# Kernel tuning notes

Measured on AMD Instinct MI355X. Metric: run time of the kernel, lower is better.

Reference implementation:

```python
import jax, jax.numpy as jnp
import numpy as np

N_NODES = 100000
D_IN = 256
D_OUT = 128
N_EDGES = 1600000
KEEP_PROB = 0.5  # tf.nn.dropout(input, 1 - 0.5) -> rate = 0.5


def setup_inputs() -> dict:
    key = jax.random.key(0)
    k_x, k_mask, k_w, k_row, k_col, k_ew = jax.random.split(key, 6)
    x = jax.random.normal(k_x, (N_NODES, D_IN), dtype=jnp.float32)
    # Deterministic scaled dropout keep-mask: Bernoulli(keep)/keep
    u = jax.random.uniform(k_mask, (N_NODES, D_IN), dtype=jnp.float32)
    dropout_mask = (u < KEEP_PROB).astype(jnp.float32) / KEEP_PROB
    kernel = jax.random.normal(k_w, (D_IN, D_OUT), dtype=jnp.float32) * (1.0 / np.sqrt(D_IN))
    edge_row = jax.random.randint(k_row, (N_EDGES,), 0, N_NODES, dtype=jnp.int32)
    edge_col = jax.random.randint(k_col, (N_EDGES,), 0, N_NODES, dtype=jnp.int32)
    edge_weight = jax.random.uniform(k_ew, (N_EDGES,), dtype=jnp.float32)
    return {"x": x, "dropout_mask": dropout_mask, "kernel": kernel,
            "edge_row": edge_row, "edge_col": edge_col, "edge_weight": edge_weight}


def reference(x, dropout_mask, kernel, edge_row, edge_col, edge_weight):
    # dropout (mask already scaled by 1/keep_prob)
    h = x * dropout_mask                      # [N, D_IN]
    # dense projection
    h = h @ kernel                            # [N, D_OUT]
    # sparse (COO) adjacency @ dense: out[r] += w_e * h[c] for each edge (r, c)
    msgs = edge_weight[:, None] * h[edge_col]            # [E, D_OUT]
    agg = jax.ops.segment_sum(msgs, edge_row, num_segments=N_NODES)  # [N, D_OUT]
    # act=True -> relu
    return jax.nn.relu(agg)
```

## Files before the change

kernel.cpp:

```cpp
#include <hip/hip_runtime.h>

constexpr int NN = 100000;
constexpr int DI = 256;
constexpr int DO = 128;
constexpr int NE = 1600000;

constexpr int BROWS = 128;
constexpr int NBK   = (NN + BROWS - 1) / BROWS;
constexpr int TILE  = 8192;
constexpr int CAP   = 2688;

typedef __bf16 bf16x8 __attribute__((ext_vector_type(8)));
typedef float  f32x4  __attribute__((ext_vector_type(4)));

__device__ inline unsigned short f2bf(float f) {
    union { float f; unsigned u; } v; v.f = f;
    return (unsigned short)((v.u + 0x7FFF + ((v.u >> 16) & 1)) >> 16);
}
__device__ inline float bf2f(unsigned u16) {
    union { unsigned u; float f; } v; v.u = u16 << 16;
    return v.f;
}

__global__ __launch_bounds__(256)
void wt_kernel(const float* __restrict__ W, unsigned short* __restrict__ Wt) {
    __shared__ float t[32][33];
    const int tx = threadIdx.x & 31, ty = threadIdx.x >> 5;
    const int k0 = (blockIdx.x >> 2) * 32, n0 = (blockIdx.x & 3) * 32;
#pragma unroll
    for (int i = 0; i < 32; i += 8)
        t[ty + i][tx] = W[(size_t)(k0 + ty + i) * DO + n0 + tx];
    __syncthreads();
#pragma unroll
    for (int i = 0; i < 32; i += 8)
        Wt[(size_t)(n0 + ty + i) * DI + k0 + tx] = f2bf(t[tx][ty + i]);
}

__global__ __launch_bounds__(256)
void gemm_kernel(const float* __restrict__ x, const float* __restrict__ mask,
                 const unsigned short* __restrict__ Wt,
                 unsigned short* __restrict__ h) {
    __shared__ unsigned short As[128][72];
    __shared__ unsigned short Bs[128][72];
    const int tid  = threadIdx.x;
    const int lane = tid & 63;
    const int w    = tid >> 6;
    const int m0   = blockIdx.x * 128;
    const int mw   = w * 32;
    const int l15  = lane & 15;
    const int l4   = lane >> 4;

    f32x4 acc[2][8];
#pragma unroll
    for (int rt = 0; rt < 2; ++rt)
#pragma unroll
        for (int ct = 0; ct < 8; ++ct) acc[rt][ct] = (f32x4){0.f, 0.f, 0.f, 0.f};

    for (int kc = 0; kc < DI; kc += 64) {
        {
            const int kl = (tid & 15) * 4;
#pragma unroll
            for (int p = 0; p < 8; ++p) {
                const int r = p * 16 + (tid >> 4);
                float4 xv = make_float4(0.f, 0.f, 0.f, 0.f);
                float4 mv = make_float4(0.f, 0.f, 0.f, 0.f);
                if (m0 + r < NN) {
                    xv = *(const float4*)(x    + (size_t)(m0 + r) * DI + kc + kl);
                    mv = *(const float4*)(mask + (size_t)(m0 + r) * DI + kc + kl);
                }
                ushort4 pk;
                pk.x = f2bf(xv.x * mv.x); pk.y = f2bf(xv.y * mv.y);
                pk.z = f2bf(xv.z * mv.z); pk.w = f2bf(xv.w * mv.w);
                *(ushort4*)&As[r][kl] = pk;
            }
        }
        {
            const int kl = (tid & 7) * 8;
#pragma unroll
            for (int p = 0; p < 4; ++p) {
                const int n = p * 32 + (tid >> 3);
                *(uint4*)&Bs[n][kl] =
                    *(const uint4*)(Wt + (size_t)n * DI + kc + kl);
            }
        }
        __syncthreads();
#pragma unroll
        for (int ks = 0; ks < 2; ++ks) {
            const int ko = ks * 32 + l4 * 8;
            bf16x8 a0 = *(const bf16x8*)&As[mw + l15][ko];
            bf16x8 a1 = *(const bf16x8*)&As[mw + 16 + l15][ko];
#pragma unroll
            for (int ct = 0; ct < 8; ++ct) {
                bf16x8 b = *(const bf16x8*)&Bs[ct * 16 + l15][ko];
                acc[0][ct] = __builtin_amdgcn_mfma_f32_16x16x32_bf16(a0, b, acc[0][ct], 0, 0, 0);
                acc[1][ct] = __builtin_amdgcn_mfma_f32_16x16x32_bf16(a1, b, acc[1][ct], 0, 0, 0);
            }
        }
        __syncthreads();
    }
#pragma unroll
    for (int rt = 0; rt < 2; ++rt)
#pragma unroll
        for (int ct = 0; ct < 8; ++ct)
#pragma unroll
            for (int reg = 0; reg < 4; ++reg) {
                const int row = m0 + mw + rt * 16 + l4 * 4 + reg;
                if (row < NN)
                    h[(size_t)row * DO + ct * 16 + l15] = f2bf(acc[rt][ct][reg]);
            }
}

__global__ __launch_bounds__(256)
void bhist_kernel(const int* __restrict__ erow, int* __restrict__ bcnt) {
    __shared__ int cnt[NBK];
    const int t = threadIdx.x;
    for (int k = t; k < NBK; k += 256) cnt[k] = 0;
    __syncthreads();
    for (int e = blockIdx.x * 256 + t; e < NE; e += 256 * 256)
        atomicAdd(&cnt[erow[e] >> 7], 1);
    __syncthreads();
    for (int k = t; k < NBK; k += 256) {
        const int c = cnt[k];
        if (c) atomicAdd(&bcnt[k], c);
    }
}

__global__ __launch_bounds__(1024)
void bscan_kernel(const int* __restrict__ bcnt, int* __restrict__ bstart,
                  int* __restrict__ bcursor) {
    __shared__ int wsum[16];
    const int t = threadIdx.x, lane = t & 63, wid = t >> 6;
    const int c = (t < NBK) ? bcnt[t] : 0;
    int v = c;
#pragma unroll
    for (int off = 1; off < 64; off <<= 1) {
        const int n = __shfl_up(v, off, 64);
        if (lane >= off) v += n;
    }
    if (lane == 63) wsum[wid] = v;
    __syncthreads();
    int p = 0;
#pragma unroll
    for (int i = 0; i < 16; ++i)
        if (i < wid) p += wsum[i];
    const int excl = p + v - c;
    if (t <= NBK) bstart[t] = excl;
    if (t < NBK)  bcursor[t] = excl;
}

__global__ __launch_bounds__(256)
void part_kernel(const int* __restrict__ erow, const int* __restrict__ ecol,
                 const float* __restrict__ ew, int* __restrict__ bcursor,
                 int2* __restrict__ csr) {
    __shared__ int cnt[NBK];
    __shared__ int base[NBK];
    const int t  = threadIdx.x;
    const int e0 = blockIdx.x * TILE;
    for (int k = t; k < NBK; k += 256) cnt[k] = 0;
    __syncthreads();
    for (int k = 0; k < TILE; k += 256) {
        const int e = e0 + k + t;
        if (e < NE) atomicAdd(&cnt[erow[e] >> 7], 1);
    }
    __syncthreads();
    for (int k = t; k < NBK; k += 256) {
        const int c = cnt[k];
        base[k] = c ? atomicAdd(&bcursor[k], c) : 0;
        cnt[k] = 0;
    }
    __syncthreads();
    for (int k = 0; k < TILE; k += 256) {
        const int e = e0 + k + t;
        if (e < NE) {
            const int row = erow[e];
            const int bk  = row >> 7;
            const int pos = atomicAdd(&cnt[bk], 1);
            int2 v;
            v.x = ((row & 127) << 17) | ecol[e];
            v.y = __float_as_int(ew[e]);
            csr[base[bk] + pos] = v;
        }
    }
}

__global__ __launch_bounds__(256)
void bgather_kernel(const unsigned short* __restrict__ h,
                    const int* __restrict__ bstart,
                    const int2* __restrict__ csr, float* __restrict__ out) {
    __shared__ int2 se[CAP];
    __shared__ int  s_cnt[BROWS];
    __shared__ int  s_start[BROWS + 1];
    __shared__ int  wtot;
    const int b = blockIdx.x, t = threadIdx.x;
    const int start = bstart[b], n = bstart[b + 1] - start;

    if (t < BROWS) s_cnt[t] = 0;
    __syncthreads();
    for (int j = t; j < n; j += 256)
        atomicAdd(&s_cnt[((unsigned)csr[start + j].x) >> 17], 1);
    __syncthreads();
    const int lane = t & 63;
    int c = 0;
    if (t < BROWS) c = s_cnt[t];
    int v = c;
#pragma unroll
    for (int off = 1; off < 64; off <<= 1) {
        const int nn = __shfl_up(v, off, 64);
        if (lane >= off) v += nn;
    }
    if (t == 63) wtot = v;
    __syncthreads();
    if (t < BROWS) {
        const int excl = v - c + (t >= 64 ? wtot : 0);
        s_start[t] = excl;
        s_cnt[t]   = excl;
    }
    if (t == 0) s_start[BROWS] = n;
    __syncthreads();
    for (int j = t; j < n; j += 256) {
        const int2 cw = csr[start + j];
        const int  pos = atomicAdd(&s_cnt[((unsigned)cw.x) >> 17], 1);
        se[pos] = cw;
    }
    __syncthreads();

    const int l16 = t & 15, g = t >> 4;
    const int row0 = b * BROWS;
#pragma unroll
    for (int rp = 0; rp < 8; ++rp) {
        const int r  = rp * 16 + g;
        const int gr = row0 + r;
        const int rs = s_start[r], re = s_start[r + 1];
        float acc[8];
#pragma unroll
        for (int i = 0; i < 8; ++i) acc[i] = 0.f;
        int j = rs;
        for (; j + 2 <= re; j += 2) {
            const int2 cw0 = se[j], cw1 = se[j + 1];
            const float w0 = __int_as_float(cw0.y);
            const float w1 = __int_as_float(cw1.y);
            const uint4 q0 = *(const uint4*)(h + (size_t)(cw0.x & 0x1FFFF) * DO + l16 * 8);
            const uint4 q1 = *(const uint4*)(h + (size_t)(cw1.x & 0x1FFFF) * DO + l16 * 8);
            const unsigned* u0 = (const unsigned*)&q0;
            const unsigned* u1 = (const unsigned*)&q1;
#pragma unroll
            for (int i = 0; i < 4; ++i) {
                acc[2 * i + 0] += w0 * bf2f(u0[i] & 0xFFFF) + w1 * bf2f(u1[i] & 0xFFFF);
                acc[2 * i + 1] += w0 * bf2f(u0[i] >> 16)    + w1 * bf2f(u1[i] >> 16);
            }
        }
        if (j < re) {
            const int2 cw = se[j];
            const float w = __int_as_float(cw.y);
            const uint4 q = *(const uint4*)(h + (size_t)(cw.x & 0x1FFFF) * DO + l16 * 8);
            const unsigned* u = (const unsigned*)&q;
#pragma unroll
            for (int i = 0; i < 4; ++i) {
                acc[2 * i + 0] += w * bf2f(u[i] & 0xFFFF);
                acc[2 * i + 1] += w * bf2f(u[i] >> 16);
            }
        }
        if (gr < NN) {
            float* op = out + (size_t)gr * DO + l16 * 8;
            *(float4*)(op + 0) = make_float4(fmaxf(acc[0], 0.f), fmaxf(acc[1], 0.f),
                                             fmaxf(acc[2], 0.f), fmaxf(acc[3], 0.f));
            *(float4*)(op + 4) = make_float4(fmaxf(acc[4], 0.f), fmaxf(acc[5], 0.f),
                                             fmaxf(acc[6], 0.f), fmaxf(acc[7], 0.f));
        }
    }
}

extern "C" void kernel_launch(void* const* d_in, const int* in_sizes, int n_in,
                              void* d_out, int out_size, void* d_ws, size_t ws_size,
                              hipStream_t stream) {
    const float* x    = (const float*)d_in[0];
    const float* mask = (const float*)d_in[1];
    const float* W    = (const float*)d_in[2];
    const int*   erow = (const int*)d_in[3];
    const int*   ecol = (const int*)d_in[4];
    const float* ew   = (const float*)d_in[5];
    float* out = (float*)d_out;

    char* p = (char*)d_ws;
    unsigned short* h  = (unsigned short*)p;  p += (size_t)NN * DO * 2;
    unsigned short* Wt = (unsigned short*)p;  p += (size_t)DO * DI * 2;
    int* bcnt    = (int*)p;                   p += 3200;
    int* bstart  = (int*)p;                   p += 3200;
    int* bcursor = (int*)p;                   p += 3200;
    int2* csr    = (int2*)p;

    hipMemsetAsync(bcnt, 0, NBK * sizeof(int), stream);

    wt_kernel<<<32, 256, 0, stream>>>(W, Wt);
    gemm_kernel<<<(NN + 127) / 128, 256, 0, stream>>>(x, mask, Wt, h);
    bhist_kernel<<<256, 256, 0, stream>>>(erow, bcnt);
    bscan_kernel<<<1, 1024, 0, stream>>>(bcnt, bstart, bcursor);
    part_kernel<<<(NE + TILE - 1) / TILE, 256, 0, stream>>>(erow, ecol, ew,
                                                            bcursor, csr);
    bgather_kernel<<<NBK, 256, 0, stream>>>(h, bstart, csr, out);
}
```

Measured before the change: 413.6 us.

## Prefetch GEMM tiles, drop histogram/scan via fixed-capacity buckets, widen gather blocks

Result: faster. 389.6 us (-5.8%).

```diff
diff --git a/kernel.cpp b/kernel.cpp
--- a/kernel.cpp
+++ b/kernel.cpp
@@ -40,39 +40,43 @@
 void gemm_kernel(const float* __restrict__ x, const float* __restrict__ mask,
                  const unsigned short* __restrict__ Wt,
                  unsigned short* __restrict__ h) {
-    __shared__ unsigned short As[128][72];
+    __shared__ unsigned short As[64][72];
     __shared__ unsigned short Bs[128][72];
     const int tid  = threadIdx.x;
     const int lane = tid & 63;
     const int w    = tid >> 6;
-    const int m0   = blockIdx.x * 128;
-    const int mw   = w * 32;
+    const int m0   = blockIdx.x * 64;
+    const int mw   = w * 16;
     const int l15  = lane & 15;
     const int l4   = lane >> 4;
 
-    f32x4 acc[2][8];
-#pragma unroll
-    for (int rt = 0; rt < 2; ++rt)
-#pragma unroll
-        for (int ct = 0; ct < 8; ++ct) acc[rt][ct] = (f32x4){0.f, 0.f, 0.f, 0.f};
+    f32x4 acc[8];
+#pragma unroll
+    for (int ct = 0; ct < 8; ++ct) acc[ct] = (f32x4){0.f, 0.f, 0.f, 0.f};
+
+    const int lr = tid >> 4;
+    const int lk = (tid & 15) * 4;
+
+    float4 xv[4], mv[4];
+    const float4 z4 = make_float4(0.f, 0.f, 0.f, 0.f);
+
+#pragma unroll
+    for (int p = 0; p < 4; ++p) {
+        const int r = m0 + p * 16 + lr;
+        if (r < NN) {
+            xv[p] = *(const float4*)(x    + (size_t)r * DI + lk);
+            mv[p] = *(const float4*)(mask + (size_t)r * DI + lk);
+        } else { xv[p] = z4; mv[p] = z4; }
+    }
 
     for (int kc = 0; kc < DI; kc += 64) {
-        {
-            const int kl = (tid & 15) * 4;
-#pragma unroll
-            for (int p = 0; p < 8; ++p) {
-                const int r = p * 16 + (tid >> 4);
-                float4 xv = make_float4(0.f, 0.f, 0.f, 0.f);
-                float4 mv = make_float4(0.f, 0.f, 0.f, 0.f);
-                if (m0 + r < NN) {
-                    xv = *(const float4*)(x    + (size_t)(m0 + r) * DI + kc + kl);
-                    mv = *(const float4*)(mask + (size_t)(m0 + r) * DI + kc + kl);
-                }
-                ushort4 pk;
-                pk.x = f2bf(xv.x * mv.x); pk.y = f2bf(xv.y * mv.y);
-                pk.z = f2bf(xv.z * mv.z); pk.w = f2bf(xv.w * mv.w);
-                *(ushort4*)&As[r][kl] = pk;
-            }
+        __syncthreads();
+#pragma unroll
+        for (int p = 0; p < 4; ++p) {
+            ushort4 pk;
+            pk.x = f2bf(xv[p].x * mv[p].x); pk.y = f2bf(xv[p].y * mv[p].y);
+            pk.z = f2bf(xv[p].z * mv[p].z); pk.w = f2bf(xv[p].w * mv[p].w);
+            *(ushort4*)&As[p * 16 + lr][lk] = pk;
         }
         {
             const int kl = (tid & 7) * 8;
@@ -83,74 +87,41 @@
                     *(const uint4*)(Wt + (size_t)n * DI + kc + kl);
             }
         }
+        if (kc + 64 < DI) {
+#pragma unroll
+            for (int p = 0; p < 4; ++p) {
+                const int r = m0 + p * 16 + lr;
+                if (r < NN) {
+                    xv[p] = *(const float4*)(x    + (size_t)r * DI + kc + 64 + lk);
+                    mv[p] = *(const float4*)(mask + (size_t)r * DI + kc + 64 + lk);
+                } else { xv[p] = z4; mv[p] = z4; }
+            }
+        }
         __syncthreads();
 #pragma unroll
         for (int ks = 0; ks < 2; ++ks) {
             const int ko = ks * 32 + l4 * 8;
-            bf16x8 a0 = *(const bf16x8*)&As[mw + l15][ko];
-            bf16x8 a1 = *(const bf16x8*)&As[mw + 16 + l15][ko];
+            const bf16x8 a0 = *(const bf16x8*)&As[mw + l15][ko];
 #pragma unroll
             for (int ct = 0; ct < 8; ++ct) {
-                bf16x8 b = *(const bf16x8*)&Bs[ct * 16 + l15][ko];
-                acc[0][ct] = __builtin_amdgcn_mfma_f32_16x16x32_bf16(a0, b, acc[0][ct], 0, 0, 0);
-                acc[1][ct] = __builtin_amdgcn_mfma_f32_16x16x32_bf16(a1, b, acc[1][ct], 0, 0, 0);
-            }
-        }
-        __syncthreads();
-    }
-#pragma unroll
-    for (int rt = 0; rt < 2; ++rt)
-#pragma unroll
-        for (int ct = 0; ct < 8; ++ct)
-#pragma unroll
-            for (int reg = 0; reg < 4; ++reg) {
-                const int row = m0 + mw + rt * 16 + l4 * 4 + reg;
-                if (row < NN)
-                    h[(size_t)row * DO + ct * 16 + l15] = f2bf(acc[rt][ct][reg]);
-            }
-}
-
-__global__ __launch_bounds__(256)
-void bhist_kernel(const int* __restrict__ erow, int* __restrict__ bcnt) {
-    __shared__ int cnt[NBK];
-    const int t = threadIdx.x;
-    for (int k = t; k < NBK; k += 256) cnt[k] = 0;
-    __syncthreads();
-    for (int e = blockIdx.x * 256 + t; e < NE; e += 256 * 256)
-        atomicAdd(&cnt[erow[e] >> 7], 1);
-    __syncthreads();
-    for (int k = t; k < NBK; k += 256) {
-        const int c = cnt[k];
-        if (c) atomicAdd(&bcnt[k], c);
-    }
-}
-
-__global__ __launch_bounds__(1024)
-void bscan_kernel(const int* __restrict__ bcnt, int* __restrict__ bstart,
-                  int* __restrict__ bcursor) {
-    __shared__ int wsum[16];
-    const int t = threadIdx.x, lane = t & 63, wid = t >> 6;
-    const int c = (t < NBK) ? bcnt[t] : 0;
-    int v = c;
-#pragma unroll
-    for (int off = 1; off < 64; off <<= 1) {
-        const int n = __shfl_up(v, off, 64);
-        if (lane >= off) v += n;
-    }
-    if (lane == 63) wsum[wid] = v;
-    __syncthreads();
-    int p = 0;
-#pragma unroll
-    for (int i = 0; i < 16; ++i)
-        if (i < wid) p += wsum[i];
-    const int excl = p + v - c;
-    if (t <= NBK) bstart[t] = excl;
-    if (t < NBK)  bcursor[t] = excl;
+                const bf16x8 b = *(const bf16x8*)&Bs[ct * 16 + l15][ko];
+                acc[ct] = __builtin_amdgcn_mfma_f32_16x16x32_bf16(a0, b, acc[ct], 0, 0, 0);
+            }
+        }
+    }
+#pragma unroll
+    for (int ct = 0; ct < 8; ++ct)
+#pragma unroll
+        for (int reg = 0; reg < 4; ++reg) {
+            const int row = m0 + mw + l4 * 4 + reg;
+            if (row < NN)
+                h[(size_t)row * DO + ct * 16 + l15] = f2bf(acc[ct][reg]);
+        }
 }
 
 __global__ __launch_bounds__(256)
 void part_kernel(const int* __restrict__ erow, const int* __restrict__ ecol,
-                 const float* __restrict__ ew, int* __restrict__ bcursor,
+                 const float* __restrict__ ew, int* __restrict__ bcnt,
                  int2* __restrict__ csr) {
     __shared__ int cnt[NBK];
     __shared__ int base[NBK];
@@ -165,7 +136,7 @@
     __syncthreads();
     for (int k = t; k < NBK; k += 256) {
         const int c = cnt[k];
-        base[k] = c ? atomicAdd(&bcursor[k], c) : 0;
+        base[k] = c ? atomicAdd(&bcnt[k], c) : 0;
         cnt[k] = 0;
     }
     __syncthreads();
@@ -178,26 +149,27 @@
             int2 v;
             v.x = ((row & 127) << 17) | ecol[e];
             v.y = __float_as_int(ew[e]);
-            csr[base[bk] + pos] = v;
-        }
-    }
-}
-
-__global__ __launch_bounds__(256)
+            csr[(size_t)bk * CAP + base[bk] + pos] = v;
+        }
+    }
+}
+
+__global__ __launch_bounds__(512)
 void bgather_kernel(const unsigned short* __restrict__ h,
-                    const int* __restrict__ bstart,
+                    const int* __restrict__ bcnt,
                     const int2* __restrict__ csr, float* __restrict__ out) {
     __shared__ int2 se[CAP];
     __shared__ int  s_cnt[BROWS];
     __shared__ int  s_start[BROWS + 1];
     __shared__ int  wtot;
     const int b = blockIdx.x, t = threadIdx.x;
-    const int start = bstart[b], n = bstart[b + 1] - start;
+    const int n = bcnt[b];
+    const int2* ebase = csr + (size_t)b * CAP;
 
     if (t < BROWS) s_cnt[t] = 0;
     __syncthreads();
-    for (int j = t; j < n; j += 256)
-        atomicAdd(&s_cnt[((unsigned)csr[start + j].x) >> 17], 1);
+    for (int j = t; j < n; j += 512)
+        atomicAdd(&s_cnt[((unsigned)ebase[j].x) >> 17], 1);
     __syncthreads();
     const int lane = t & 63;
     int c = 0;
@@ -217,8 +189,8 @@
     }
     if (t == 0) s_start[BROWS] = n;
     __syncthreads();
-    for (int j = t; j < n; j += 256) {
-        const int2 cw = csr[start + j];
+    for (int j = t; j < n; j += 512) {
+        const int2 cw  = ebase[j];
         const int  pos = atomicAdd(&s_cnt[((unsigned)cw.x) >> 17], 1);
         se[pos] = cw;
     }
@@ -227,8 +199,8 @@
     const int l16 = t & 15, g = t >> 4;
     const int row0 = b * BROWS;
 #pragma unroll
-    for (int rp = 0; rp < 8; ++rp) {
-        const int r  = rp * 16 + g;
+    for (int rp = 0; rp < 4; ++rp) {
+        const int r  = rp * 32 + g;
         const int gr = row0 + r;
         const int rs = s_start[r], re = s_start[r + 1];
         float acc[8];
@@ -284,18 +256,14 @@
     char* p = (char*)d_ws;
     unsigned short* h  = (unsigned short*)p;  p += (size_t)NN * DO * 2;
     unsigned short* Wt = (unsigned short*)p;  p += (size_t)DO * DI * 2;
-    int* bcnt    = (int*)p;                   p += 3200;
-    int* bstart  = (int*)p;                   p += 3200;
-    int* bcursor = (int*)p;                   p += 3200;
-    int2* csr    = (int2*)p;
+    int* bcnt = (int*)p;                      p += 3200;
+    int2* csr = (int2*)p;
 
     hipMemsetAsync(bcnt, 0, NBK * sizeof(int), stream);
 
     wt_kernel<<<32, 256, 0, stream>>>(W, Wt);
-    gemm_kernel<<<(NN + 127) / 128, 256, 0, stream>>>(x, mask, Wt, h);
-    bhist_kernel<<<256, 256, 0, stream>>>(erow, bcnt);
-    bscan_kernel<<<1, 1024, 0, stream>>>(bcnt, bstart, bcursor);
+    gemm_kernel<<<(NN + 63) / 64, 256, 0, stream>>>(x, mask, Wt, h);
     part_kernel<<<(NE + TILE - 1) / TILE, 256, 0, stream>>>(erow, ecol, ew,
-                                                            bcursor, csr);
-    bgather_kernel<<<NBK, 256, 0, stream>>>(h, bstart, csr, out);
-}
+                                                            bcnt, csr);
+    bgather_kernel<<<NBK, 512, 0, stream>>>(h, bcnt, csr, out);
+}
```
